# Performance work log

Hardware: AMD Instinct MI355X
Metric: run time of the kernel (lower is better)

## Reference

```python
import jax, jax.numpy as jnp
import numpy as np


def setup_inputs() -> dict:
    key = jax.random.key(0)
    k1, k2 = jax.random.split(key)
    B, Lq, Lk, D = 4, 4096, 4096, 512
    query = jax.random.normal(k1, (B, Lq, D), dtype=jnp.float32)
    value = jax.random.normal(k2, (B, Lk, D), dtype=jnp.float32)
    return {"query": query, "value": value}


def reference(query, value):
    # score: [B, Lq, Lk] = query @ value^T (unscaled, unmasked)
    score = jnp.einsum('bqd,bkd->bqk', query, value)
    attn = jax.nn.softmax(score, axis=-1)
    # context: [B, Lq, D]
    context = jnp.einsum('bqk,bkd->bqd', attn, value)
    return (context, attn)
```

## Files before the change

kernel.cpp:

```cpp
#include <hip/hip_runtime.h>
#include <cstddef>
#include <cstdint>

typedef unsigned short u16;

constexpr int BATCH = 4;
constexpr int Lq = 4096;
constexpr int Lk = 4096;
constexpr int D  = 512;

constexpr int BM = 128, BN = 128, BK = 32;
constexpr int LDA = 40;

using bf16x8 = __attribute__((ext_vector_type(8))) short;
using f32x4  = __attribute__((ext_vector_type(4))) float;

__device__ inline u16 f32_to_bf16_rne(float x) {
    uint32_t u = __builtin_bit_cast(uint32_t, x);
    u += 0x7fff + ((u >> 16) & 1);
    return (u16)(u >> 16);
}
__device__ inline float bf16_bits_to_f32(u16 h) {
    uint32_t u = ((uint32_t)h) << 16;
    return __builtin_bit_cast(float, u);
}
__device__ inline void split2(float x, float y, uint32_t& hi, uint32_t& lo) {
    u16 hx = f32_to_bf16_rne(x);
    u16 hy = f32_to_bf16_rne(y);
    u16 lx = f32_to_bf16_rne(x - bf16_bits_to_f32(hx));
    u16 ly = f32_to_bf16_rne(y - bf16_bits_to_f32(hy));
    hi = (uint32_t)hx | ((uint32_t)hy << 16);
    lo = (uint32_t)lx | ((uint32_t)ly << 16);
}
__device__ inline uint32_t pack2_bf16(float x, float y) {
    return (uint32_t)f32_to_bf16_rne(x) | ((uint32_t)f32_to_bf16_rne(y) << 16);
}
__device__ inline void gld16(const u16* g, u16* l) {
    __builtin_amdgcn_global_load_lds(
        (const __attribute__((address_space(1))) void*)g,
        (__attribute__((address_space(3))) void*)l, 16, 0, 0);
}
__device__ inline f32x4 mfma16(bf16x8 a, bf16x8 b, f32x4 c) {
    return __builtin_amdgcn_mfma_f32_16x16x32_bf16(a, b, c, 0, 0, 0);
}

__global__ __launch_bounds__(256)
void split_qv_bf16(const float* __restrict__ Q, const float* __restrict__ V,
                   u16* __restrict__ Qhi, u16* __restrict__ Qlo,
                   u16* __restrict__ Vhi, u16* __restrict__ Vlo, int n4)
{
    int i = blockIdx.x * 256 + threadIdx.x;
    const float* src;
    u16 *hi, *lo;
    if (i < n4) { src = Q; hi = Qhi; lo = Qlo; }
    else        { src = V; hi = Vhi; lo = Vlo; i -= n4; }
    const float4 v = ((const float4*)src)[i];
    uint2 h, l;
    split2(v.x, v.y, h.x, l.x);
    split2(v.z, v.w, h.y, l.y);
    ((uint2*)hi)[i] = h;
    ((uint2*)lo)[i] = l;
}

__global__ __launch_bounds__(256)
void transpose_v_bf16(const float* __restrict__ V, u16* __restrict__ VT)
{
    __shared__ float tile[32][33];
    const int b = blockIdx.z;
    const float* in = V + (size_t)b * Lk * D;
    u16* out = VT + (size_t)b * D * Lk;
    const int lk0 = blockIdx.x * 32;
    const int d0  = blockIdx.y * 32;
    const int c  = threadIdx.x & 31;
    const int r0 = threadIdx.x >> 5;
    #pragma unroll
    for (int i = 0; i < 4; ++i) {
        const int r = r0 + 8 * i;
        tile[r][c] = in[(size_t)(lk0 + r) * D + d0 + c];
    }
    __syncthreads();
    #pragma unroll
    for (int i = 0; i < 4; ++i) {
        const int r = r0 + 8 * i;
        out[(size_t)(d0 + r) * Lk + lk0 + c] = f32_to_bf16_rne(tile[c][r]);
    }
}

__global__ __launch_bounds__(512, 2)
void gemm1_8p(const u16* __restrict__ Qhi, const u16* __restrict__ Qlo,
              const u16* __restrict__ Vhi, const u16* __restrict__ Vlo,
              float* __restrict__ Sg)
{
    constexpr int K  = D;
    constexpr int NT = K / 32;
    __shared__ u16 lds[2 * 4 * 8192];

    const int b = blockIdx.z;
    const u16* Ah = Qhi + (size_t)b * Lq * K;
    const u16* Al = Qlo + (size_t)b * Lq * K;
    const u16* Bh = Vhi + (size_t)b * Lk * K;
    const u16* Bl = Vlo + (size_t)b * Lk * K;
    float* C = Sg + (size_t)b * Lq * Lk;

    const int m0 = blockIdx.y * 256;
    const int n0 = blockIdx.x * 256;
    const int t = threadIdx.x, lane = t & 63, w = t >> 6;
    const int wm = (w >> 2) * 128, wn = (w & 3) * 64;
    const int fr = lane & 15, fq = lane >> 4;

    const int cg   = (lane & 3) ^ ((lane >> 3) & 3);
    const int rsub = lane >> 2;
    const int offA0 = (m0 + w * 32 + rsub) * K + cg * 8;
    const int offA1 = offA0 + 16 * K;
    const int offB0 = (n0 + w * 32 + rsub) * K + cg * 8;
    const int offB1 = offB0 + 16 * K;
    const int ch = w * 1024;

    const int swzc = fq ^ ((fr >> 1) & 3);
    const int aRd = (wm + fr) * 64 + swzc * 16;
    const int bRd = (wn + fr) * 64 + swzc * 16;

    f32x4 acc[8][4] = {};
    bf16x8 aH[4], aL[4], bH[4], bL[4];

    {
        u16* a = &lds[ch];
        gld16(Ah + offA0, a);
        gld16(Ah + offA1, a + 512);
        gld16(Al + offA0, a + 8192);
        gld16(Al + offA1, a + 8192 + 512);
        u16* v = &lds[16384 + ch];
        gld16(Bh + offB0, v);
        gld16(Bh + offB1, v + 512);
        gld16(Bl + offB0, v + 8192);
        gld16(Bl + offB1, v + 8192 + 512);
    }
    asm volatile("s_waitcnt vmcnt(0)" ::: "memory");
    __builtin_amdgcn_s_barrier();
    __builtin_amdgcn_sched_barrier(0);

    for (int kt = 0; kt < NT; ++kt) {
        const int cur = kt & 1;
        const char* ls = (const char*)lds + cur * 65536;
        const int kn = (kt + 1) * 32;
        const int nb = (cur ^ 1) * 32768;

        #pragma unroll
        for (int m = 0; m < 4; ++m) {
            aH[m] = *(const bf16x8*)(ls + aRd + m * 1024);
            aL[m] = *(const bf16x8*)(ls + 16384 + aRd + m * 1024);
        }
        #pragma unroll
        for (int n = 0; n < 2; ++n) {
            bH[n] = *(const bf16x8*)(ls + 32768 + bRd + n * 1024);
            bL[n] = *(const bf16x8*)(ls + 49152 + bRd + n * 1024);
        }
        if (kt < NT - 1) {
            u16* a = &lds[nb + ch];
            gld16(Ah + offA0 + kn, a);
            gld16(Ah + offA1 + kn, a + 512);
            gld16(Al + offA0 + kn, a + 8192);
            gld16(Al + offA1 + kn, a + 8192 + 512);
        }
        __builtin_amdgcn_s_barrier();
        asm volatile("s_waitcnt lgkmcnt(0)" ::: "memory");
        __builtin_amdgcn_sched_barrier(0);
        __builtin_amdgcn_s_setprio(1);
        #pragma unroll
        for (int m = 0; m < 4; ++m)
            #pragma unroll
            for (int n = 0; n < 2; ++n) {
                acc[m][n] = mfma16(aH[m], bH[n], acc[m][n]);
                acc[m][n] = mfma16(aH[m], bL[n], acc[m][n]);
                acc[m][n] = mfma16(aL[m], bH[n], acc[m][n]);
            }
        __builtin_amdgcn_s_setprio(0);
        __builtin_amdgcn_s_barrier();
        __builtin_amdgcn_sched_barrier(0);

        #pragma unroll
        for (int n = 2; n < 4; ++n) {
            bH[n] = *(const bf16x8*)(ls + 32768 + bRd + n * 1024);
            bL[n] = *(const bf16x8*)(ls + 49152 + bRd + n * 1024);
        }
        if (kt < NT - 1) {
            u16* v = &lds[nb + 16384 + ch];
            gld16(Bh + offB0 + kn, v);
            gld16(Bh + offB1 + kn, v + 512);
            gld16(Bl + offB0 + kn, v + 8192);
            gld16(Bl + offB1 + kn, v + 8192 + 512);
        }
        __builtin_amdgcn_s_barrier();
        asm volatile("s_waitcnt lgkmcnt(0)" ::: "memory");
        __builtin_amdgcn_sched_barrier(0);
        __builtin_amdgcn_s_setprio(1);
        #pragma unroll
        for (int m = 0; m < 4; ++m)
            #pragma unroll
            for (int n = 2; n < 4; ++n) {
                acc[m][n] = mfma16(aH[m], bH[n], acc[m][n]);
                acc[m][n] = mfma16(aH[m], bL[n], acc[m][n]);
                acc[m][n] = mfma16(aL[m], bH[n], acc[m][n]);
            }
        __builtin_amdgcn_s_setprio(0);
        __builtin_amdgcn_s_barrier();
        __builtin_amdgcn_sched_barrier(0);

        #pragma unroll
        for (int m = 0; m < 4; ++m) {
            aH[m] = *(const bf16x8*)(ls + 4096 + aRd + m * 1024);
            aL[m] = *(const bf16x8*)(ls + 16384 + 4096 + aRd + m * 1024);
        }
        __builtin_amdgcn_s_barrier();
        asm volatile("s_waitcnt lgkmcnt(0)" ::: "memory");
        __builtin_amdgcn_sched_barrier(0);
        __builtin_amdgcn_s_setprio(1);
        #pragma unroll
        for (int m = 0; m < 4; ++m)
            #pragma unroll
            for (int n = 0; n < 2; ++n) {
                acc[4 + m][n] = mfma16(aH[m], bH[n], acc[4 + m][n]);
                acc[4 + m][n] = mfma16(aH[m], bL[n], acc[4 + m][n]);
                acc[4 + m][n] = mfma16(aL[m], bH[n], acc[4 + m][n]);
            }
        __builtin_amdgcn_s_setprio(0);
        __builtin_amdgcn_s_barrier();
        __builtin_amdgcn_sched_barrier(0);

        __builtin_amdgcn_s_setprio(1);
        #pragma unroll
        for (int m = 0; m < 4; ++m)
            #pragma unroll
            for (int n = 2; n < 4; ++n) {
                acc[4 + m][n] = mfma16(aH[m], bH[n], acc[4 + m][n]);
                acc[4 + m][n] = mfma16(aH[m], bL[n], acc[4 + m][n]);
                acc[4 + m][n] = mfma16(aL[m], bH[n], acc[4 + m][n]);
            }
        __builtin_amdgcn_s_setprio(0);
        asm volatile("s_waitcnt vmcnt(0)" ::: "memory");
        __builtin_amdgcn_s_barrier();
        __builtin_amdgcn_sched_barrier(0);
    }

    const int rowb = m0 + wm + fq * 4;
    const int colb = n0 + wn + fr;
    #pragma unroll
    for (int mi = 0; mi < 8; ++mi)
        #pragma unroll
        for (int ni = 0; ni < 4; ++ni)
            #pragma unroll
            for (int r = 0; r < 4; ++r)
                C[(size_t)(rowb + mi * 16 + r) * Lk + colb + ni * 16] = acc[mi][ni][r];
}

__global__ __launch_bounds__(256)
void row_stats(const float* __restrict__ S, float* __restrict__ rowM,
               float* __restrict__ rowI)
{
    const size_t row = (size_t)blockIdx.x * 4 + (threadIdx.x >> 6);
    const int l = threadIdx.x & 63;
    const float* p = S + row * (size_t)Lk;

    float4 v[16];
    #pragma unroll
    for (int j = 0; j < 16; ++j) v[j] = ((const float4*)p)[l + j * 64];

    float m = -3.0e38f;
    #pragma unroll
    for (int j = 0; j < 16; ++j)
        m = fmaxf(m, fmaxf(fmaxf(v[j].x, v[j].y), fmaxf(v[j].z, v[j].w)));
    #pragma unroll
    for (int off = 32; off > 0; off >>= 1) m = fmaxf(m, __shfl_xor(m, off));

    float s = 0.f;
    #pragma unroll
    for (int j = 0; j < 16; ++j) {
        s += __expf(v[j].x - m);
        s += __expf(v[j].y - m);
        s += __expf(v[j].z - m);
        s += __expf(v[j].w - m);
    }
    #pragma unroll
    for (int off = 32; off > 0; off >>= 1) s += __shfl_xor(s, off);

    if (l == 0) {
        rowM[row] = m;
        rowI[row] = 1.0f / s;
    }
}

__global__ __launch_bounds__(512, 4)
void fused_pv(float* __restrict__ S, const u16* __restrict__ VTg,
              float* __restrict__ ctx, const float* __restrict__ rowM,
              const float* __restrict__ rowI)
{
    constexpr int NT = Lk / 64;
    __shared__ u16 sB[512 * 64];
    __shared__ u16 sA[32 * 64];

    const int i = blockIdx.x;
    const int b = (i >> 1) & 3;
    const int rt = ((i >> 3) << 1) | (i & 1);
    const int m0 = rt * 32;

    float* Srow = S + ((size_t)b * Lq + m0) * Lk;
    const u16* VT = VTg + (size_t)b * (size_t)D * Lk;
    float* C = ctx + ((size_t)b * Lq + m0) * D;

    const int t = threadIdx.x, lane = t & 63, w = t >> 6;
    const int fr = lane & 15, fq = lane >> 4;

    const int srow = t >> 4;
    const int sk = (t & 15) * 4;
    const float mrow = rowM[(size_t)b * Lq + m0 + srow];
    const float inv  = rowI[(size_t)b * Lq + m0 + srow];
    const int aw = srow * 64 + (((sk >> 3) ^ (srow & 7)) * 8) + (sk & 4);

    const int vrow = w * 8 + (lane >> 3);
    const int vck = (lane & 7) ^ (lane >> 3);
    const int swc = fr & 7;

    f32x4 acc[2][4] = {};

    for (int kt = 0; kt < NT; ++kt) {
        const int k0 = kt * 64;
        if (kt) __syncthreads();

        #pragma unroll
        for (int j = 0; j < 8; ++j)
            gld16(VT + (size_t)(j * 64 + vrow) * Lk + k0 + vck * 8,
                  &sB[(j * 512 + w * 64) * 8]);

        float4 v = *(const float4*)(Srow + (size_t)srow * Lk + k0 + sk);
        v.x = __expf(v.x - mrow) * inv;
        v.y = __expf(v.y - mrow) * inv;
        v.z = __expf(v.z - mrow) * inv;
        v.w = __expf(v.w - mrow) * inv;
        *(float4*)(Srow + (size_t)srow * Lk + k0 + sk) = v;
        uint2 h;
        h.x = pack2_bf16(v.x, v.y);
        h.y = pack2_bf16(v.z, v.w);
        *(uint2*)&sA[aw] = h;

        __syncthreads();

        #pragma unroll
        for (int ks = 0; ks < 2; ++ks) {
            const int pc = (ks * 4 + fq) ^ swc;
            bf16x8 af[2], bf[4];
            #pragma unroll
            for (int x = 0; x < 2; ++x)
                af[x] = *(const bf16x8*)&sA[(x * 16 + fr) * 64 + pc * 8];
            #pragma unroll
            for (int x = 0; x < 4; ++x)
                bf[x] = *(const bf16x8*)&sB[(w * 64 + x * 16 + fr) * 64 + pc * 8];
            #pragma unroll
            for (int mi = 0; mi < 2; ++mi)
                #pragma unroll
                for (int ni = 0; ni < 4; ++ni)
                    acc[mi][ni] = mfma16(af[mi], bf[ni], acc[mi][ni]);
        }
    }

    #pragma unroll
    for (int mi = 0; mi < 2; ++mi)
        #pragma unroll
        for (int ni = 0; ni < 4; ++ni)
            #pragma unroll
            for (int r = 0; r < 4; ++r)
                C[(size_t)(mi * 16 + fq * 4 + r) * D + w * 64 + ni * 16 + fr] =
                    acc[mi][ni][r];
}

__global__ __launch_bounds__(256)
void softmax_wave(float* __restrict__ S, u16* __restrict__ Pb)
{
    const size_t row = (size_t)blockIdx.x * 4 + (threadIdx.x >> 6);
    const int l = threadIdx.x & 63;
    float* p = S + row * (size_t)Lk;

    float4 v[16];
    #pragma unroll
    for (int j = 0; j < 16; ++j) v[j] = ((const float4*)p)[l + j * 64];

    float m = -3.0e38f;
    #pragma unroll
    for (int j = 0; j < 16; ++j)
        m = fmaxf(m, fmaxf(fmaxf(v[j].x, v[j].y), fmaxf(v[j].z, v[j].w)));
    #pragma unroll
    for (int off = 32; off > 0; off >>= 1) m = fmaxf(m, __shfl_xor(m, off));

    float s = 0.f;
    #pragma unroll
    for (int j = 0; j < 16; ++j) {
        v[j].x = __expf(v[j].x - m); s += v[j].x;
        v[j].y = __expf(v[j].y - m); s += v[j].y;
        v[j].z = __expf(v[j].z - m); s += v[j].z;
        v[j].w = __expf(v[j].w - m); s += v[j].w;
    }
    #pragma unroll
    for (int off = 32; off > 0; off >>= 1) s += __shfl_xor(s, off);

    const float inv = 1.0f / s;
    u16* prow = Pb ? Pb + row * (size_t)Lk : nullptr;
    #pragma unroll
    for (int j = 0; j < 16; ++j) {
        v[j].x *= inv; v[j].y *= inv; v[j].z *= inv; v[j].w *= inv;
        ((float4*)p)[l + j * 64] = v[j];
        if (prow) {
            ushort4 h = make_ushort4(f32_to_bf16_rne(v[j].x), f32_to_bf16_rne(v[j].y),
                                     f32_to_bf16_rne(v[j].z), f32_to_bf16_rne(v[j].w));
            ((ushort4*)prow)[l + j * 64] = h;
        }
    }
}

__global__ __launch_bounds__(256, 2)
void gemm1_r2(const float* __restrict__ Qg, const float* __restrict__ Vg,
              float* __restrict__ Sg)
{
    constexpr int K = D;
    __shared__ alignas(16) u16 sAhi[BM * LDA];
    __shared__ alignas(16) u16 sAlo[BM * LDA];
    __shared__ alignas(16) u16 sBhi[BN * LDA];
    __shared__ alignas(16) u16 sBlo[BN * LDA];

    const int b = blockIdx.z;
    const float* A  = Qg + (size_t)b * Lq * D;
    const float* Bp = Vg + (size_t)b * Lk * D;
    float* C = Sg + (size_t)b * Lq * Lk;

    const int m0 = blockIdx.y * BM;
    const int n0 = blockIdx.x * BN;
    const int t = threadIdx.x, lane = t & 63, wave = t >> 6;
    const int wm = (wave >> 1) * 64, wn = (wave & 1) * 64;
    const int fr = lane & 15, fq = lane >> 4;
    const int sm = t >> 3, sc = t & 7;

    f32x4 acc[4][4] = {};

    for (int k0 = 0; k0 < K; k0 += BK) {
        if (k0) __syncthreads();
        #pragma unroll
        for (int i = 0; i < 4; ++i) {
            const int m = sm + 32 * i;
            const float4 va = *(const float4*)(A  + (size_t)(m0 + m) * K + k0 + sc * 4);
            const float4 vb = *(const float4*)(Bp + (size_t)(n0 + m) * K + k0 + sc * 4);
            uint2 h, l;
            split2(va.x, va.y, h.x, l.x);
            split2(va.z, va.w, h.y, l.y);
            *(uint2*)&sAhi[m * LDA + sc * 4] = h;
            *(uint2*)&sAlo[m * LDA + sc * 4] = l;
            split2(vb.x, vb.y, h.x, l.x);
            split2(vb.z, vb.w, h.y, l.y);
            *(uint2*)&sBhi[m * LDA + sc * 4] = h;
            *(uint2*)&sBlo[m * LDA + sc * 4] = l;
        }
        __syncthreads();

        bf16x8 ah[4], al[4], bh[4], bl[4];
        #pragma unroll
        for (int x = 0; x < 4; ++x) {
            ah[x] = *(const bf16x8*)&sAhi[(wm + x * 16 + fr) * LDA + fq * 8];
            al[x] = *(const bf16x8*)&sAlo[(wm + x * 16 + fr) * LDA + fq * 8];
            bh[x] = *(const bf16x8*)&sBhi[(wn + x * 16 + fr) * LDA + fq * 8];
            bl[x] = *(const bf16x8*)&sBlo[(wn + x * 16 + fr) * LDA + fq * 8];
        }
        #pragma unroll
        for (int mi = 0; mi < 4; ++mi)
            #pragma unroll
            for (int ni = 0; ni < 4; ++ni) {
                acc[mi][ni] = __builtin_amdgcn_mfma_f32_16x16x32_bf16(ah[mi], bh[ni], acc[mi][ni], 0, 0, 0);
                acc[mi][ni] = __builtin_amdgcn_mfma_f32_16x16x32_bf16(ah[mi], bl[ni], acc[mi][ni], 0, 0, 0);
                acc[mi][ni] = __builtin_amdgcn_mfma_f32_16x16x32_bf16(al[mi], bh[ni], acc[mi][ni], 0, 0, 0);
            }
    }

    #pragma unroll
    for (int mi = 0; mi < 4; ++mi)
        #pragma unroll
        for (int ni = 0; ni < 4; ++ni)
            #pragma unroll
            for (int r = 0; r < 4; ++r) {
                const int row = m0 + wm + mi * 16 + fq * 4 + r;
                const int col = n0 + wn + ni * 16 + fr;
                C[(size_t)row * Lk + col] = acc[mi][ni][r];
            }
}

__global__ __launch_bounds__(256, 2)
void gemm2_r2(const float* __restrict__ Pg, const u16* __restrict__ VTg,
              float* __restrict__ Cg)
{
    constexpr int K = Lk;
    constexpr int N = D;
    __shared__ alignas(16) u16 sA[BM * LDA];
    __shared__ alignas(16) u16 sB[BN * LDA];

    const int b = blockIdx.z;
    const float* A  = Pg  + (size_t)b * Lq * Lk;
    const u16*   Bp = VTg + (size_t)b * (size_t)D * Lk;
    float* C = Cg + (size_t)b * Lq * D;

    const int m0 = blockIdx.y * BM;
    const int n0 = blockIdx.x * BN;
    const int t = threadIdx.x, lane = t & 63, wave = t >> 6;
    const int wm = (wave >> 1) * 64, wn = (wave & 1) * 64;
    const int fr = lane & 15, fq = lane >> 4;
    const int sm = t >> 3, sc = t & 7;
    const int bn = t >> 2, bc = t & 3;

    f32x4 acc[4][4] = {};

    for (int k0 = 0; k0 < K; k0 += BK) {
        if (k0) __syncthreads();
        #pragma unroll
        for (int i = 0; i < 4; ++i) {
            const int m = sm + 32 * i;
            const float4 va = *(const float4*)(A + (size_t)(m0 + m) * K + k0 + sc * 4);
            uint2 h;
            h.x = pack2_bf16(va.x, va.y);
            h.y = pack2_bf16(va.z, va.w);
            *(uint2*)&sA[m * LDA + sc * 4] = h;
        }
        #pragma unroll
        for (int i = 0; i < 2; ++i) {
            const int n = bn + 64 * i;
            const bf16x8 vb = *(const bf16x8*)(Bp + (size_t)(n0 + n) * K + k0 + bc * 8);
            *(bf16x8*)&sB[n * LDA + bc * 8] = vb;
        }
        __syncthreads();

        bf16x8 af[4], bf[4];
        #pragma unroll
        for (int x = 0; x < 4; ++x) {
            af[x] = *(const bf16x8*)&sA[(wm + x * 16 + fr) * LDA + fq * 8];
            bf[x] = *(const bf16x8*)&sB[(wn + x * 16 + fr) * LDA + fq * 8];
        }
        #pragma unroll
        for (int mi = 0; mi < 4; ++mi)
            #pragma unroll
            for (int ni = 0; ni < 4; ++ni)
                acc[mi][ni] = __builtin_amdgcn_mfma_f32_16x16x32_bf16(af[mi], bf[ni], acc[mi][ni], 0, 0, 0);
    }

    #pragma unroll
    for (int mi = 0; mi < 4; ++mi)
        #pragma unroll
        for (int ni = 0; ni < 4; ++ni)
            #pragma unroll
            for (int r = 0; r < 4; ++r) {
                const int row = m0 + wm + mi * 16 + fq * 4 + r;
                const int col = n0 + wn + ni * 16 + fr;
                C[(size_t)row * N + col] = acc[mi][ni][r];
            }
}

extern "C" void kernel_launch(void* const* d_in, const int* in_sizes, int n_in,
                              void* d_out, int out_size, void* d_ws, size_t ws_size,
                              hipStream_t stream)
{
    const float* Q = (const float*)d_in[0];
    const float* V = (const float*)d_in[1];
    float* ctx  = (float*)d_out;
    float* attn = (float*)d_out + (size_t)BATCH * Lq * D;

    constexpr size_t NQ = (size_t)BATCH * Lq * D;
    constexpr size_t NP = (size_t)BATCH * Lq * Lk;
    const size_t need = (5 * NQ + NP) * sizeof(u16);

    if (ws_size >= need) {
        u16* Qhi = (u16*)d_ws;
        u16* Qlo = Qhi + NQ;
        u16* Vhi = Qlo + NQ;
        u16* Vlo = Vhi + NQ;
        u16* VT  = Vlo + NQ;
        u16* Pb  = VT  + NQ;

        float* rowM = (float*)Pb;
        float* rowI = rowM + (size_t)BATCH * Lq;

        const int n4 = (int)(NQ / 4);
        split_qv_bf16<<<dim3(2 * n4 / 256), 256, 0, stream>>>(Q, V, Qhi, Qlo, Vhi, Vlo, n4);
        transpose_v_bf16<<<dim3(Lk / 32, D / 32, BATCH), 256, 0, stream>>>(V, VT);
        gemm1_8p<<<dim3(Lk / 256, Lq / 256, BATCH), 512, 0, stream>>>(Qhi, Qlo, Vhi, Vlo, attn);
        row_stats<<<dim3(BATCH * Lq / 4), 256, 0, stream>>>(attn, rowM, rowI);
        fused_pv<<<dim3(512), 512, 0, stream>>>(attn, VT, ctx, rowM, rowI);
    } else {
        u16* VT = (u16*)d_ws;
        transpose_v_bf16<<<dim3(Lk / 32, D / 32, BATCH), 256, 0, stream>>>(V, VT);
        gemm1_r2<<<dim3(Lk / BN, Lq / BM, BATCH), 256, 0, stream>>>(Q, V, attn);
        softmax_wave<<<dim3(BATCH * Lq / 4), 256, 0, stream>>>(attn, nullptr);
        gemm2_r2<<<dim3(D / BN, Lq / BM, BATCH), 256, 0, stream>>>(attn, VT, ctx);
    }
}
```

Before: 770.1 us.

## Fuse row stats into PV kernel with double-buffered tiles and 64-row blocks

Removes the separate row_stats kernel: each PV block now computes row max and sum for its 64 rows itself, then runs the exp-normalize, write-back and P·V GEMM. The PV loop gains double-buffered shared memory for V^T and P tiles, prefetching the next tile's scores and V during the MFMAs. Block height doubles to 64 rows, so 256 blocks run instead of 512, which halves V reuse traffic but lowers parallelism to one block per CU on 256 CUs. Occupancy drops because of the larger LDS use, and the extra launch and rowM/rowI round-trip go away.

```diff
diff --git a/kernel.cpp b/kernel.cpp
--- a/kernel.cpp
+++ b/kernel.cpp
@@ -253,55 +253,18 @@
                 C[(size_t)(rowb + mi * 16 + r) * Lk + colb + ni * 16] = acc[mi][ni][r];
 }
 
-__global__ __launch_bounds__(256)
-void row_stats(const float* __restrict__ S, float* __restrict__ rowM,
-               float* __restrict__ rowI)
-{
-    const size_t row = (size_t)blockIdx.x * 4 + (threadIdx.x >> 6);
-    const int l = threadIdx.x & 63;
-    const float* p = S + row * (size_t)Lk;
-
-    float4 v[16];
-    #pragma unroll
-    for (int j = 0; j < 16; ++j) v[j] = ((const float4*)p)[l + j * 64];
-
-    float m = -3.0e38f;
-    #pragma unroll
-    for (int j = 0; j < 16; ++j)
-        m = fmaxf(m, fmaxf(fmaxf(v[j].x, v[j].y), fmaxf(v[j].z, v[j].w)));
-    #pragma unroll
-    for (int off = 32; off > 0; off >>= 1) m = fmaxf(m, __shfl_xor(m, off));
-
-    float s = 0.f;
-    #pragma unroll
-    for (int j = 0; j < 16; ++j) {
-        s += __expf(v[j].x - m);
-        s += __expf(v[j].y - m);
-        s += __expf(v[j].z - m);
-        s += __expf(v[j].w - m);
-    }
-    #pragma unroll
-    for (int off = 32; off > 0; off >>= 1) s += __shfl_xor(s, off);
-
-    if (l == 0) {
-        rowM[row] = m;
-        rowI[row] = 1.0f / s;
-    }
-}
-
-__global__ __launch_bounds__(512, 4)
-void fused_pv(float* __restrict__ S, const u16* __restrict__ VTg,
-              float* __restrict__ ctx, const float* __restrict__ rowM,
-              const float* __restrict__ rowI)
+__global__ __launch_bounds__(512, 2)
+void fused_spv(float* __restrict__ S, const u16* __restrict__ VTg,
+               float* __restrict__ ctx)
 {
     constexpr int NT = Lk / 64;
-    __shared__ u16 sB[512 * 64];
-    __shared__ u16 sA[32 * 64];
+    __shared__ u16 sB[2][512 * 64];
+    __shared__ u16 sA[2][64 * 72];
+    __shared__ float mro[64], iro[64];
 
     const int i = blockIdx.x;
-    const int b = (i >> 1) & 3;
-    const int rt = ((i >> 3) << 1) | (i & 1);
-    const int m0 = rt * 32;
+    const int b = i >> 6;
+    const int m0 = (i & 63) * 64;
 
     float* Srow = S + ((size_t)b * Lq + m0) * Lk;
     const u16* VT = VTg + (size_t)b * (size_t)D * Lk;
@@ -310,60 +273,114 @@
     const int t = threadIdx.x, lane = t & 63, w = t >> 6;
     const int fr = lane & 15, fq = lane >> 4;
 
-    const int srow = t >> 4;
-    const int sk = (t & 15) * 4;
-    const float mrow = rowM[(size_t)b * Lq + m0 + srow];
-    const float inv  = rowI[(size_t)b * Lq + m0 + srow];
-    const int aw = srow * 64 + (((sk >> 3) ^ (srow & 7)) * 8) + (sk & 4);
-
     const int vrow = w * 8 + (lane >> 3);
-    const int vck = (lane & 7) ^ (lane >> 3);
-    const int swc = fr & 7;
-
-    f32x4 acc[2][4] = {};
+    const int vck  = (lane & 7) ^ (lane >> 3);
+    const int swc  = fr & 7;
+
+    const int sr = t >> 3, so = t & 7;
+
+    #pragma unroll
+    for (int j = 0; j < 8; ++j)
+        gld16(VT + (size_t)(j * 64 + vrow) * Lk + vck * 8,
+              &sB[0][(j * 512 + w * 64) * 8]);
+
+    #pragma unroll 1
+    for (int rr = 0; rr < 8; ++rr) {
+        const int r = w * 8 + rr;
+        const float* p = Srow + (size_t)r * Lk;
+        float4 v[16];
+        #pragma unroll
+        for (int j = 0; j < 16; ++j) v[j] = ((const float4*)p)[lane + j * 64];
+        float m = -3.0e38f;
+        #pragma unroll
+        for (int j = 0; j < 16; ++j)
+            m = fmaxf(m, fmaxf(fmaxf(v[j].x, v[j].y), fmaxf(v[j].z, v[j].w)));
+        #pragma unroll
+        for (int off = 32; off > 0; off >>= 1) m = fmaxf(m, __shfl_xor(m, off));
+        float s = 0.f;
+        #pragma unroll
+        for (int j = 0; j < 16; ++j) {
+            s += __expf(v[j].x - m);
+            s += __expf(v[j].y - m);
+            s += __expf(v[j].z - m);
+            s += __expf(v[j].w - m);
+        }
+        #pragma unroll
+        for (int off = 32; off > 0; off >>= 1) s += __shfl_xor(s, off);
+        if (lane == 0) { mro[r] = m; iro[r] = 1.0f / s; }
+    }
+    __syncthreads();
+    const float mr_ = mro[sr], ir_ = iro[sr];
+
+    float4 sv0, sv1;
+    {
+        const float4 a = *(const float4*)(Srow + (size_t)sr * Lk + so * 8);
+        const float4 c2 = *(const float4*)(Srow + (size_t)sr * Lk + so * 8 + 4);
+        sv0.x = __expf(a.x - mr_) * ir_;  sv0.y = __expf(a.y - mr_) * ir_;
+        sv0.z = __expf(a.z - mr_) * ir_;  sv0.w = __expf(a.w - mr_) * ir_;
+        sv1.x = __expf(c2.x - mr_) * ir_; sv1.y = __expf(c2.y - mr_) * ir_;
+        sv1.z = __expf(c2.z - mr_) * ir_; sv1.w = __expf(c2.w - mr_) * ir_;
+        uint4 hq;
+        hq.x = pack2_bf16(sv0.x, sv0.y); hq.y = pack2_bf16(sv0.z, sv0.w);
+        hq.z = pack2_bf16(sv1.x, sv1.y); hq.w = pack2_bf16(sv1.z, sv1.w);
+        *(uint4*)&sA[0][sr * 72 + so * 8] = hq;
+    }
+    __syncthreads();
+
+    f32x4 acc[4][4] = {};
 
     for (int kt = 0; kt < NT; ++kt) {
+        const int cur = kt & 1, nxt = cur ^ 1;
         const int k0 = kt * 64;
-        if (kt) __syncthreads();
-
-        #pragma unroll
-        for (int j = 0; j < 8; ++j)
-            gld16(VT + (size_t)(j * 64 + vrow) * Lk + k0 + vck * 8,
-                  &sB[(j * 512 + w * 64) * 8]);
-
-        float4 v = *(const float4*)(Srow + (size_t)srow * Lk + k0 + sk);
-        v.x = __expf(v.x - mrow) * inv;
-        v.y = __expf(v.y - mrow) * inv;
-        v.z = __expf(v.z - mrow) * inv;
-        v.w = __expf(v.w - mrow) * inv;
-        *(float4*)(Srow + (size_t)srow * Lk + k0 + sk) = v;
-        uint2 h;
-        h.x = pack2_bf16(v.x, v.y);
-        h.y = pack2_bf16(v.z, v.w);
-        *(uint2*)&sA[aw] = h;
-
-        __syncthreads();
-
+
+        *(float4*)(Srow + (size_t)sr * Lk + k0 + so * 8)     = sv0;
+        *(float4*)(Srow + (size_t)sr * Lk + k0 + so * 8 + 4) = sv1;
+
+        float4 la, lb;
+        if (kt + 1 < NT) {
+            const int kn = k0 + 64;
+            #pragma unroll
+            for (int j = 0; j < 8; ++j)
+                gld16(VT + (size_t)(j * 64 + vrow) * Lk + kn + vck * 8,
+                      &sB[nxt][(j * 512 + w * 64) * 8]);
+            la = *(const float4*)(Srow + (size_t)sr * Lk + kn + so * 8);
+            lb = *(const float4*)(Srow + (size_t)sr * Lk + kn + so * 8 + 4);
+        }
+
+        __builtin_amdgcn_s_setprio(1);
         #pragma unroll
         for (int ks = 0; ks < 2; ++ks) {
-            const int pc = (ks * 4 + fq) ^ swc;
-            bf16x8 af[2], bf[4];
-            #pragma unroll
-            for (int x = 0; x < 2; ++x)
-                af[x] = *(const bf16x8*)&sA[(x * 16 + fr) * 64 + pc * 8];
+            const int oc = ks * 4 + fq;
+            bf16x8 af[4], bf[4];
             #pragma unroll
             for (int x = 0; x < 4; ++x)
-                bf[x] = *(const bf16x8*)&sB[(w * 64 + x * 16 + fr) * 64 + pc * 8];
-            #pragma unroll
-            for (int mi = 0; mi < 2; ++mi)
+                af[x] = *(const bf16x8*)&sA[cur][(x * 16 + fr) * 72 + oc * 8];
+            #pragma unroll
+            for (int x = 0; x < 4; ++x)
+                bf[x] = *(const bf16x8*)&sB[cur][(w * 64 + x * 16 + fr) * 64 + (oc ^ swc) * 8];
+            #pragma unroll
+            for (int mi = 0; mi < 4; ++mi)
                 #pragma unroll
                 for (int ni = 0; ni < 4; ++ni)
                     acc[mi][ni] = mfma16(af[mi], bf[ni], acc[mi][ni]);
         }
-    }
-
-    #pragma unroll
-    for (int mi = 0; mi < 2; ++mi)
+        __builtin_amdgcn_s_setprio(0);
+
+        if (kt + 1 < NT) {
+            sv0.x = __expf(la.x - mr_) * ir_;  sv0.y = __expf(la.y - mr_) * ir_;
+            sv0.z = __expf(la.z - mr_) * ir_;  sv0.w = __expf(la.w - mr_) * ir_;
+            sv1.x = __expf(lb.x - mr_) * ir_;  sv1.y = __expf(lb.y - mr_) * ir_;
+            sv1.z = __expf(lb.z - mr_) * ir_;  sv1.w = __expf(lb.w - mr_) * ir_;
+            uint4 hq;
+            hq.x = pack2_bf16(sv0.x, sv0.y); hq.y = pack2_bf16(sv0.z, sv0.w);
+            hq.z = pack2_bf16(sv1.x, sv1.y); hq.w = pack2_bf16(sv1.z, sv1.w);
+            *(uint4*)&sA[nxt][sr * 72 + so * 8] = hq;
+        }
+        __syncthreads();
+    }
+
+    #pragma unroll
+    for (int mi = 0; mi < 4; ++mi)
         #pragma unroll
         for (int ni = 0; ni < 4; ++ni)
             #pragma unroll
@@ -575,17 +592,12 @@
         u16* Vhi = Qlo + NQ;
         u16* Vlo = Vhi + NQ;
         u16* VT  = Vlo + NQ;
-        u16* Pb  = VT  + NQ;
-
-        float* rowM = (float*)Pb;
-        float* rowI = rowM + (size_t)BATCH * Lq;
 
         const int n4 = (int)(NQ / 4);
         split_qv_bf16<<<dim3(2 * n4 / 256), 256, 0, stream>>>(Q, V, Qhi, Qlo, Vhi, Vlo, n4);
         transpose_v_bf16<<<dim3(Lk / 32, D / 32, BATCH), 256, 0, stream>>>(V, VT);
         gemm1_8p<<<dim3(Lk / 256, Lq / 256, BATCH), 512, 0, stream>>>(Qhi, Qlo, Vhi, Vlo, attn);
-        row_stats<<<dim3(BATCH * Lq / 4), 256, 0, stream>>>(attn, rowM, rowI);
-        fused_pv<<<dim3(512), 512, 0, stream>>>(attn, VT, ctx, rowM, rowI);
+        fused_spv<<<dim3(256), 512, 0, stream>>>(attn, VT, ctx);
     } else {
         u16* VT = (u16*)d_ws;
         transpose_v_bf16<<<dim3(Lk / 32, D / 32, BATCH), 256, 0, stream>>>(V, VT);
```

Result: faster. 747.8 us (-2.9%).
